# Optimization experiments

Measured on AMD Instinct MI355X. Metric: run time of the kernel, lower is better.

Reference implementation:

```python
import jax, jax.numpy as jnp
import numpy as np

NNODES = 8192
K = 512
NEG_SLOPE = 0.01  # torch F.leaky_relu default
EPS = 1e-12       # torch F.normalize default eps


def setup_inputs() -> dict:
    key = jax.random.key(0)
    kx, kp = jax.random.split(key)
    x = jax.random.normal(kx, (NNODES, K), dtype=jnp.float32)
    # xavier_uniform init for proto (nnodes, k)
    bound = float(np.sqrt(6.0 / (NNODES + K)))
    proto = jax.random.uniform(kp, (NNODES, K), dtype=jnp.float32,
                               minval=-bound, maxval=bound)
    return {"x": x, "proto": proto}


def reference(x, proto):
    # In-place no_grad step in torch: proto <- l2norm(proto), rows unit-norm.
    norm = jnp.sqrt(jnp.sum(proto * proto, axis=1, keepdims=True))
    pn = proto / jnp.maximum(norm, EPS)  # (nnodes, k), unit rows
    # cosine_similarity over all pairs == pn @ pn.T since rows are unit-norm.
    # This fuses torch's (nnodes, nnodes, k) broadcast into one GEMM.
    sim = jnp.einsum('ik,jk->ij', pn, pn)  # (nnodes, nnodes)
    return jnp.where(sim >= 0, sim, NEG_SLOPE * sim)
```

## Files before the change

### kernel.cpp

```cpp
#include <hip/hip_runtime.h>
#include <stdint.h>

#define NN 8192
#define KD 512
#define BM 128
#define BK 32
#define NTILE (NN / BM)
#define NTRI (NTILE * (NTILE + 1) / 2)
#define NKT (KD / BK)

typedef __bf16 bf16;
typedef __bf16 bf16x8 __attribute__((ext_vector_type(8)));
typedef float f32x4 __attribute__((ext_vector_type(4)));

__global__ __launch_bounds__(256) void rownorm_kernel(const float* __restrict__ proto,
                                                      bf16* __restrict__ pn) {
    const int row  = blockIdx.x * 4 + (threadIdx.x >> 6);
    const int lane = threadIdx.x & 63;
    const float4* src = (const float4*)(proto + (size_t)row * KD) + lane * 2;
    const float4 v0 = src[0];
    const float4 v1 = src[1];
    float s = v0.x*v0.x + v0.y*v0.y + v0.z*v0.z + v0.w*v0.w
            + v1.x*v1.x + v1.y*v1.y + v1.z*v1.z + v1.w*v1.w;
#pragma unroll
    for (int off = 32; off; off >>= 1) s += __shfl_xor(s, off);
    const float inv = 1.0f / fmaxf(sqrtf(s), 1e-12f);
    bf16x8 o;
    o[0] = (bf16)(v0.x*inv); o[1] = (bf16)(v0.y*inv);
    o[2] = (bf16)(v0.z*inv); o[3] = (bf16)(v0.w*inv);
    o[4] = (bf16)(v1.x*inv); o[5] = (bf16)(v1.y*inv);
    o[6] = (bf16)(v1.z*inv); o[7] = (bf16)(v1.w*inv);
    *(bf16x8*)(pn + (size_t)row * KD + lane * 8) = o;
}

__device__ __forceinline__ void gload_lds16(const bf16* g, bf16* l) {
    __builtin_amdgcn_global_load_lds(
        (const __attribute__((address_space(1))) void*)g,
        (__attribute__((address_space(3))) void*)l, 16, 0, 0);
}

__device__ __forceinline__ float lrelu(float v) {
    return (v >= 0.0f) ? v : 0.01f * v;
}

__global__ __launch_bounds__(256, 4) void gemm_sym_kernel(const bf16* __restrict__ P,
                                                          float* __restrict__ C) {
    __shared__ __align__(16) unsigned char smem[33280];
    bf16*  sA = (bf16*)smem;
    bf16*  sB = (bf16*)(smem + 16384);
    float* sE = (float*)smem;
    float* sM = (float*)smem;

    const int bid = blockIdx.x;
    const int swz = (bid & 7) * (NTRI / 8) + (bid >> 3);
    int tm = 0, rem = swz;
    while (rem >= NTILE - tm) { rem -= NTILE - tm; ++tm; }
    const int tn = tm + rem;

    const int tid  = threadIdx.x;
    const int w    = tid >> 6;
    const int lane = tid & 63;
    const int wr = w >> 1;
    const int rowA0 = tm * BM;
    const int rowB0 = tn * BM;
    const int wm = wr * 64;
    const int wn = (w & 1) * 64;
    const int rr = lane & 15;
    const int h  = lane >> 4;

    const int chunk0 = w * 128 + lane;
    const bf16* g0 = P + (size_t)(chunk0 >> 2) * KD + (chunk0 & 3) * 8;
    const size_t offA = (size_t)rowA0 * KD;
    const size_t offB = (size_t)rowB0 * KD;
    const int ldsOff0 = w * 1024;
    const int ldsOff1 = w * 1024 + 512;

    f32x4 acc[4][4] = {};

#define STAGE(buf, kt)                                                        \
    do {                                                                      \
        gload_lds16(g0 + offA + (kt),           sA + (buf) * 4096 + ldsOff0); \
        gload_lds16(g0 + offA + 16 * KD + (kt), sA + (buf) * 4096 + ldsOff1); \
        gload_lds16(g0 + offB + (kt),           sB + (buf) * 4096 + ldsOff0); \
        gload_lds16(g0 + offB + 16 * KD + (kt), sB + (buf) * 4096 + ldsOff1); \
    } while (0)

#define COMPUTE(buf)                                                          \
    do {                                                                      \
        const bf16* ra_ = sA + (buf) * 4096;                                  \
        const bf16* rb_ = sB + (buf) * 4096;                                  \
        bf16x8 af[4], bfr[4];                                                 \
        _Pragma("unroll")                                                     \
        for (int m = 0; m < 4; ++m)                                           \
            af[m] = *(const bf16x8*)(ra_ + (wm + m * 16 + rr) * 32 + h * 8);  \
        _Pragma("unroll")                                                     \
        for (int n = 0; n < 4; ++n)                                           \
            bfr[n] = *(const bf16x8*)(rb_ + (wn + n * 16 + rr) * 32 + h * 8); \
        _Pragma("unroll")                                                     \
        for (int m = 0; m < 4; ++m)                                           \
            _Pragma("unroll")                                                 \
            for (int n = 0; n < 4; ++n)                                       \
                acc[m][n] = __builtin_amdgcn_mfma_f32_16x16x32_bf16(          \
                    af[m], bfr[n], acc[m][n], 0, 0, 0);                       \
    } while (0)

    STAGE(0, 0);
    __syncthreads();

#pragma unroll
    for (int t = 0; t < NKT; ++t) {
        if (t < NKT - 1) STAGE((t + 1) & 1, (t + 1) * BK);
        COMPUTE(t & 1);
        if (t < NKT - 1) __syncthreads();
    }

    const int cr = h * 4;
    const int cc = rr;

#define LGKM0_BAR()                                                   \
    do {                                                              \
        asm volatile("s_waitcnt lgkmcnt(0)" ::: "memory");            \
        __builtin_amdgcn_s_barrier();                                 \
    } while (0)

#pragma unroll
    for (int H = 0; H < 2; ++H) {
        LGKM0_BAR();
        if (wr == H) {
#pragma unroll
            for (int m = 0; m < 4; ++m)
#pragma unroll
                for (int n = 0; n < 4; ++n)
#pragma unroll
                    for (int r = 0; r < 4; ++r)
                        sE[(m * 16 + cr + r) * 129 + wn + n * 16 + cc] =
                            lrelu(acc[m][n][r]);
        }
        LGKM0_BAR();

#pragma unroll
        for (int k = 0; k < 8; ++k) {
            const int seg = tid + k * 256;
            const int lr  = seg >> 5;
            const int c4  = (seg & 31) * 4;
            const f32x4 v = *(const f32x4*)&sE[lr * 129 + c4];
            __builtin_nontemporal_store(
                v, (f32x4*)&C[(size_t)(rowA0 + H * 64 + lr) * NN + rowB0 + c4]);
        }
        LGKM0_BAR();

        if (wr == H) {
#pragma unroll
            for (int m = 0; m < 4; ++m)
#pragma unroll
                for (int n = 0; n < 4; ++n) {
                    f32x4 tv;
                    tv[0] = lrelu(acc[m][n][0]);
                    tv[1] = lrelu(acc[m][n][1]);
                    tv[2] = lrelu(acc[m][n][2]);
                    tv[3] = lrelu(acc[m][n][3]);
                    *(f32x4*)&sM[(wn + n * 16 + cc) * 65 + m * 16 + cr] = tv;
                }
        }
        LGKM0_BAR();

        if (tm != tn) {
#pragma unroll
            for (int rd = 0; rd < 8; ++rd) {
                const int j  = (tid >> 4) + rd * 16;
                const int i0 = (tid & 15) * 4;
                const f32x4 v = *(const f32x4*)&sM[j * 65 + i0];
                __builtin_nontemporal_store(
                    v, (f32x4*)&C[(size_t)(rowB0 + j) * NN + rowA0 + H * 64 + i0]);
            }
        }
    }
#undef STAGE
#undef COMPUTE
#undef LGKM0_BAR
}

extern "C" void kernel_launch(void* const* d_in, const int* in_sizes, int n_in,
                              void* d_out, int out_size, void* d_ws, size_t ws_size,
                              hipStream_t stream) {
    const float* proto = (const float*)d_in[1];
    float* C  = (float*)d_out;
    bf16* pn  = (bf16*)d_ws;

    rownorm_kernel<<<dim3(NN / 4), dim3(256), 0, stream>>>(proto, pn);
    gemm_sym_kernel<<<dim3(NTRI), dim3(256), 0, stream>>>(pn, C);
}
```

Measured before the change: 96.39 us.

## Process two symmetric tiles per block, overlapping first tile's stores with second GEMM

Each block now computes a pair of upper-triangular output tiles. While the second tile's K loop runs, the first tile's leaky-ReLU results are written straight from registers to both the tile and its mirror position, with manual vmcnt waits so loads and stores overlap. The second tile uses the existing LDS-transposed epilogue, but with ordinary stores instead of nontemporal ones. This hides output write time behind MFMA work. The costs are a second accumulator set, which raises register pressure (occupancy hint lowered from 4 to 3), and uncoalesced scalar or strided stores for the first tile.

```diff
diff --git a/kernel.cpp b/kernel.cpp
--- a/kernel.cpp
+++ b/kernel.cpp
@@ -7,6 +7,7 @@
 #define BK 32
 #define NTILE (NN / BM)
 #define NTRI (NTILE * (NTILE + 1) / 2)
+#define NPAIR (NTRI / 2)
 #define NKT (KD / BK)
 
 typedef __bf16 bf16;
@@ -43,49 +44,61 @@
     return (v >= 0.0f) ? v : 0.01f * v;
 }
 
-__global__ __launch_bounds__(256, 4) void gemm_sym_kernel(const bf16* __restrict__ P,
-                                                          float* __restrict__ C) {
+__global__ __launch_bounds__(256, 3) void gemm_sym_pair_kernel(const bf16* __restrict__ P,
+                                                               float* __restrict__ C) {
     __shared__ __align__(16) unsigned char smem[33280];
     bf16*  sA = (bf16*)smem;
     bf16*  sB = (bf16*)(smem + 16384);
     float* sE = (float*)smem;
     float* sM = (float*)smem;
 
-    const int bid = blockIdx.x;
-    const int swz = (bid & 7) * (NTRI / 8) + (bid >> 3);
-    int tm = 0, rem = swz;
-    while (rem >= NTILE - tm) { rem -= NTILE - tm; ++tm; }
-    const int tn = tm + rem;
+    const int bid  = blockIdx.x;
+    const int swzp = (bid & 7) * (NPAIR / 8) + (bid >> 3);
+    const int s0   = swzp * 2;
+    int tm0 = 0, rem = s0;
+    while (rem >= NTILE - tm0) { rem -= NTILE - tm0; ++tm0; }
+    const int tn0 = tm0 + rem;
+    const int tm1 = (tn0 + 1 < NTILE) ? tm0 : tm0 + 1;
+    const int tn1 = (tn0 + 1 < NTILE) ? tn0 + 1 : tm0 + 1;
 
     const int tid  = threadIdx.x;
     const int w    = tid >> 6;
     const int lane = tid & 63;
-    const int wr = w >> 1;
-    const int rowA0 = tm * BM;
-    const int rowB0 = tn * BM;
-    const int wm = wr * 64;
+    const int wm = (w >> 1) * 64;
     const int wn = (w & 1) * 64;
     const int rr = lane & 15;
     const int h  = lane >> 4;
+    const int cr = h * 4;
+    const int cc = rr;
+
+    const int rowA0 = tm0 * BM, rowB0 = tn0 * BM;
+    const int rowA1 = tm1 * BM, rowB1 = tn1 * BM;
 
     const int chunk0 = w * 128 + lane;
     const bf16* g0 = P + (size_t)(chunk0 >> 2) * KD + (chunk0 & 3) * 8;
-    const size_t offA = (size_t)rowA0 * KD;
-    const size_t offB = (size_t)rowB0 * KD;
+    const size_t offA0 = (size_t)rowA0 * KD, offB0 = (size_t)rowB0 * KD;
+    const size_t offA1 = (size_t)rowA1 * KD, offB1 = (size_t)rowB1 * KD;
     const int ldsOff0 = w * 1024;
     const int ldsOff1 = w * 1024 + 512;
 
-    f32x4 acc[4][4] = {};
-
-#define STAGE(buf, kt)                                                        \
+#define VMCNT(n) asm volatile("s_waitcnt vmcnt(" #n ")" ::: "memory")
+
+#define LDS_FENCE_BAR()                                               \
+    do {                                                              \
+        asm volatile("s_waitcnt lgkmcnt(0)" ::: "memory");            \
+        __builtin_amdgcn_sched_barrier(0);                            \
+        __builtin_amdgcn_s_barrier();                                 \
+    } while (0)
+
+#define STAGEX(buf, kt, oA, oB)                                               \
     do {                                                                      \
-        gload_lds16(g0 + offA + (kt),           sA + (buf) * 4096 + ldsOff0); \
-        gload_lds16(g0 + offA + 16 * KD + (kt), sA + (buf) * 4096 + ldsOff1); \
-        gload_lds16(g0 + offB + (kt),           sB + (buf) * 4096 + ldsOff0); \
-        gload_lds16(g0 + offB + 16 * KD + (kt), sB + (buf) * 4096 + ldsOff1); \
+        gload_lds16(g0 + (oA) + (kt),           sA + (buf) * 4096 + ldsOff0); \
+        gload_lds16(g0 + (oA) + 16 * KD + (kt), sA + (buf) * 4096 + ldsOff1); \
+        gload_lds16(g0 + (oB) + (kt),           sB + (buf) * 4096 + ldsOff0); \
+        gload_lds16(g0 + (oB) + 16 * KD + (kt), sB + (buf) * 4096 + ldsOff1); \
     } while (0)
 
-#define COMPUTE(buf)                                                          \
+#define COMPUTEX(buf, accv)                                                   \
     do {                                                                      \
         const bf16* ra_ = sA + (buf) * 4096;                                  \
         const bf16* rb_ = sB + (buf) * 4096;                                  \
@@ -100,32 +113,54 @@
         for (int m = 0; m < 4; ++m)                                           \
             _Pragma("unroll")                                                 \
             for (int n = 0; n < 4; ++n)                                       \
-                acc[m][n] = __builtin_amdgcn_mfma_f32_16x16x32_bf16(          \
-                    af[m], bfr[n], acc[m][n], 0, 0, 0);                       \
+                accv[m][n] = __builtin_amdgcn_mfma_f32_16x16x32_bf16(         \
+                    af[m], bfr[n], accv[m][n], 0, 0, 0);                      \
     } while (0)
 
-    STAGE(0, 0);
+    f32x4 acc0[4][4] = {};
+    STAGEX(0, 0, offA0, offB0);
     __syncthreads();
-
 #pragma unroll
     for (int t = 0; t < NKT; ++t) {
-        if (t < NKT - 1) STAGE((t + 1) & 1, (t + 1) * BK);
-        COMPUTE(t & 1);
+        if (t < NKT - 1) STAGEX((t + 1) & 1, (t + 1) * BK, offA0, offB0);
+        COMPUTEX(t & 1, acc0);
         if (t < NKT - 1) __syncthreads();
     }
 
-    const int cr = h * 4;
-    const int cc = rr;
-
-#define LGKM0_BAR()                                                   \
-    do {                                                              \
-        asm volatile("s_waitcnt lgkmcnt(0)" ::: "memory");            \
-        __builtin_amdgcn_s_barrier();                                 \
-    } while (0)
-
+    f32x4 acc1[4][4] = {};
+    STAGEX(0, 0, offA1, offB1);
+    LDS_FENCE_BAR();
+
+#pragma unroll
+    for (int t = 0; t < NKT; ++t) {
+        if (t < NKT - 1) STAGEX((t + 1) & 1, (t + 1) * BK, offA1, offB1);
+        if (t == 0)            VMCNT(4);
+        else if (t < NKT - 1)  VMCNT(9);
+        else                   VMCNT(5);
+        __builtin_amdgcn_s_barrier();
+        COMPUTEX(t & 1, acc1);
+        {
+            const int m = t >> 2, r = t & 3;
+#pragma unroll
+            for (int n = 0; n < 4; ++n)
+                C[(size_t)(rowA0 + wm + m * 16 + cr + r) * NN
+                  + (rowB0 + wn + n * 16 + cc)] = lrelu(acc0[m][n][r]);
+            const int mm = t & 3, nn = t >> 2;
+            f32x4 mv;
+            mv[0] = lrelu(acc0[mm][nn][0]);
+            mv[1] = lrelu(acc0[mm][nn][1]);
+            mv[2] = lrelu(acc0[mm][nn][2]);
+            mv[3] = lrelu(acc0[mm][nn][3]);
+            *(f32x4*)&C[(size_t)(rowB0 + wn + nn * 16 + cc) * NN
+                        + (rowA0 + wm + mm * 16 + cr)] = mv;
+        }
+        if (t < NKT - 1) LDS_FENCE_BAR();
+    }
+
+    const int wr = w >> 1;
 #pragma unroll
     for (int H = 0; H < 2; ++H) {
-        LGKM0_BAR();
+        LDS_FENCE_BAR();
         if (wr == H) {
 #pragma unroll
             for (int m = 0; m < 4; ++m)
@@ -134,50 +169,46 @@
 #pragma unroll
                     for (int r = 0; r < 4; ++r)
                         sE[(m * 16 + cr + r) * 129 + wn + n * 16 + cc] =
-                            lrelu(acc[m][n][r]);
-        }
-        LGKM0_BAR();
-
+                            lrelu(acc1[m][n][r]);
+        }
+        LDS_FENCE_BAR();
 #pragma unroll
         for (int k = 0; k < 8; ++k) {
             const int seg = tid + k * 256;
             const int lr  = seg >> 5;
             const int c4  = (seg & 31) * 4;
             const f32x4 v = *(const f32x4*)&sE[lr * 129 + c4];
-            __builtin_nontemporal_store(
-                v, (f32x4*)&C[(size_t)(rowA0 + H * 64 + lr) * NN + rowB0 + c4]);
-        }
-        LGKM0_BAR();
-
+            *(f32x4*)&C[(size_t)(rowA1 + H * 64 + lr) * NN + rowB1 + c4] = v;
+        }
+        LDS_FENCE_BAR();
         if (wr == H) {
 #pragma unroll
             for (int m = 0; m < 4; ++m)
 #pragma unroll
                 for (int n = 0; n < 4; ++n) {
                     f32x4 tv;
-                    tv[0] = lrelu(acc[m][n][0]);
-                    tv[1] = lrelu(acc[m][n][1]);
-                    tv[2] = lrelu(acc[m][n][2]);
-                    tv[3] = lrelu(acc[m][n][3]);
+                    tv[0] = lrelu(acc1[m][n][0]);
+                    tv[1] = lrelu(acc1[m][n][1]);
+                    tv[2] = lrelu(acc1[m][n][2]);
+                    tv[3] = lrelu(acc1[m][n][3]);
                     *(f32x4*)&sM[(wn + n * 16 + cc) * 65 + m * 16 + cr] = tv;
                 }
         }
-        LGKM0_BAR();
-
-        if (tm != tn) {
+        LDS_FENCE_BAR();
+        if (tm1 != tn1) {
 #pragma unroll
             for (int rd = 0; rd < 8; ++rd) {
                 const int j  = (tid >> 4) + rd * 16;
                 const int i0 = (tid & 15) * 4;
                 const f32x4 v = *(const f32x4*)&sM[j * 65 + i0];
-                __builtin_nontemporal_store(
-                    v, (f32x4*)&C[(size_t)(rowB0 + j) * NN + rowA0 + H * 64 + i0]);
+                *(f32x4*)&C[(size_t)(rowB1 + j) * NN + rowA1 + H * 64 + i0] = v;
             }
         }
     }
-#undef STAGE
-#undef COMPUTE
-#undef LGKM0_BAR
+#undef STAGEX
+#undef COMPUTEX
+#undef VMCNT
+#undef LDS_FENCE_BAR
 }
 
 extern "C" void kernel_launch(void* const* d_in, const int* in_sizes, int n_in,
@@ -188,5 +219,5 @@
     bf16* pn  = (bf16*)d_ws;
 
     rownorm_kernel<<<dim3(NN / 4), dim3(256), 0, stream>>>(proto, pn);
-    gemm_sym_kernel<<<dim3(NTRI), dim3(256), 0, stream>>>(pn, C);
-}
+    gemm_sym_pair_kernel<<<dim3(NPAIR), dim3(256), 0, stream>>>(pn, C);
+}
```

After: 113.6 us. 1.18x slower.
